# Performance work log

Hardware: AMD Instinct MI355X
Metric: run time of the kernel (lower is better)

Reference implementation:

```python
import jax, jax.numpy as jnp
import numpy as np

B, L, C, H, DK, MAXREL = 4, 1024, 768, 12, 64, 7
NEG = -2.0 ** 15  # masked_fill value


def _rel_pos_table(L, m):
    # abs distance, compressed logarithmically beyond m, clipped to [0, 2m]
    i = jnp.arange(L, dtype=jnp.float32)
    d = jnp.abs(i[:, None] - i[None, :])
    comp = m + jnp.log2(jnp.maximum(d - m, 1.0))
    d = jnp.where(d > m, comp, d)
    return jnp.clip(d, 0, 2 * m).astype(jnp.int32)  # [L, L]


def setup_inputs() -> dict:
    key = jax.random.key(0)
    ks = jax.random.split(key, 16)
    s = 0.02
    return {
        "qx": jax.random.normal(ks[0], (B, L, C), jnp.float32),
        "kx": jax.random.normal(ks[1], (B, L, C), jnp.float32),
        "vx": jax.random.normal(ks[2], (B, L, C), jnp.float32),
        "WQ_w": jax.random.normal(ks[3], (C, H * DK), jnp.float32) * s,
        "WQ_b": jnp.zeros((H * DK,), jnp.float32),
        "WK_w": jax.random.normal(ks[4], (C, H * DK), jnp.float32) * s,
        "WK_b": jnp.zeros((H * DK,), jnp.float32),
        "WV_w": jax.random.normal(ks[5], (C, H * DK), jnp.float32) * s,
        "WV_b": jnp.zeros((H * DK,), jnp.float32),
        "WO_w": jax.random.normal(ks[6], (H * DK, C), jnp.float32) * s,
        "WO_b": jnp.zeros((C,), jnp.float32),
        "embK": jax.random.normal(ks[7], (2 * MAXREL + 1, H), jnp.float32),
        "embB": jax.random.normal(ks[8], (2 * MAXREL + 1, H), jnp.float32) * s,
        "preScores": jax.random.normal(ks[9], (B, H, L, L), jnp.float32) * 0.1,
        "maskPAD": jnp.ones((B, L, L), jnp.int32),
    }


def reference(qx, kx, vx, WQ_w, WQ_b, WK_w, WK_b, WV_w, WV_b, WO_w, WO_b,
              embK, embB, preScores, maskPAD):
    q = (qx @ WQ_w + WQ_b).reshape(B, L, H, DK).transpose(0, 2, 1, 3)  # [B,H,L,dk]
    k = (kx @ WK_w + WK_b).reshape(B, L, H, DK).transpose(0, 2, 1, 3)
    v = (vx @ WV_w + WV_b).reshape(B, L, H, DK).transpose(0, 2, 1, 3)

    scores = jnp.einsum('bhid,bhjd->bhij', q, k) / np.sqrt(DK).astype(np.float32)

    tab = _rel_pos_table(L, MAXREL)                 # [L, L] int
    relK = jnp.transpose(embK[tab], (2, 1, 0))      # [H, L, L] (torch transpose(0,-1))
    relB = jnp.transpose(embB[tab], (2, 1, 0))
    scores = scores * relK[None] + relB[None]

    scores = scores + preScores
    scores = jnp.where((maskPAD == 0)[:, None, :, :], jnp.float32(NEG), scores)

    alpha = jax.nn.softmax(scores, axis=-1)         # dropout is identity in eval
    z = jnp.einsum('bhij,bhjd->bhid', alpha, v)     # [B,H,L,dk]
    z = z.transpose(0, 2, 1, 3).reshape(B, L, H * DK)
    z = z @ WO_w + WO_b
    return (z, scores)
```

## Files before the change

### kernel.cpp

```cpp
#include <hip/hip_runtime.h>
#include <stdint.h>


typedef __attribute__((ext_vector_type(4))) float f32x4;
typedef __attribute__((ext_vector_type(4))) int   i32x4;
typedef __attribute__((ext_vector_type(8))) short short8;
typedef __attribute__((ext_vector_type(4))) unsigned int u32x4;
typedef __attribute__((ext_vector_type(2))) unsigned int u32x2;

__device__ __forceinline__ unsigned short f2bf(float f) {
  unsigned int u = __float_as_uint(f);
  u += 0x7fffu + ((u >> 16) & 1u);
  return (unsigned short)(u >> 16);
}

__global__ __launch_bounds__(256) void conv_x_kernel(
    const float* __restrict__ qx, const float* __restrict__ kx,
    const float* __restrict__ vx, unsigned short* __restrict__ out) {
  int v = blockIdx.x * 256 + threadIdx.x;
  int mat = v / 786432;
  int r = v - mat * 786432;
  const float* src = (mat == 0) ? qx : (mat == 1) ? kx : vx;
  f32x4 x = ((const f32x4*)src)[r];
  union { unsigned short s[4]; u32x2 u; } o;
  o.s[0] = f2bf(x[0]); o.s[1] = f2bf(x[1]); o.s[2] = f2bf(x[2]); o.s[3] = f2bf(x[3]);
  ((u32x2*)out)[v] = o.u;
}

__global__ __launch_bounds__(256) void conv_mask_kernel(
    const int* __restrict__ m, unsigned int* __restrict__ out) {
  int w = blockIdx.x * 256 + threadIdx.x;
  const int* src = m + (size_t)w * 32;
  unsigned int bits = 0u;
#pragma unroll
  for (int c = 0; c < 8; c++) {
    i32x4 v = *(const i32x4*)&src[c * 4];
#pragma unroll
    for (int r = 0; r < 4; r++)
      bits |= (v[r] != 0 ? 1u : 0u) << (c * 4 + r);
  }
  out[w] = bits;
}

__global__ __launch_bounds__(256) void conv_w_kernel(
    const float* __restrict__ w0, const float* __restrict__ w1,
    const float* __restrict__ w2, const float* __restrict__ w3,
    unsigned short* __restrict__ out) {
  __shared__ float T[64][65];
  int bx = blockIdx.x;
  int mat = bx / 144; int t2 = bx - mat * 144;
  int kt = t2 / 12, nt = t2 - kt * 12;
  int k0 = kt * 64, n0 = nt * 64;
  const float* W = (mat == 0) ? w0 : (mat == 1) ? w1 : (mat == 2) ? w2 : w3;
  unsigned short* WT = out + (size_t)mat * 589824;
  int t = threadIdx.x;
  int lr = t >> 4;
  int lc = (t & 15) * 4;
#pragma unroll
  for (int p = 0; p < 4; p++) {
    int row = p * 16 + lr;
    f32x4 x = *(const f32x4*)&W[(size_t)(k0 + row) * 768 + n0 + lc];
    T[lc + 0][row] = x[0]; T[lc + 1][row] = x[1];
    T[lc + 2][row] = x[2]; T[lc + 3][row] = x[3];
  }
  __syncthreads();
#pragma unroll
  for (int p = 0; p < 4; p++) {
    int row = p * 16 + lr;
    union { unsigned short s[4]; u32x2 u; } o;
    o.s[0] = f2bf(T[row][lc + 0]); o.s[1] = f2bf(T[row][lc + 1]);
    o.s[2] = f2bf(T[row][lc + 2]); o.s[3] = f2bf(T[row][lc + 3]);
    *(u32x2*)&WT[(size_t)(n0 + row) * 768 + k0 + lc] = o.u;
  }
}

__global__ __launch_bounds__(256, 2) void qkv_gemm_kernel(
    const unsigned short* __restrict__ xbf, const unsigned short* __restrict__ wt,
    const float* __restrict__ bq, const float* __restrict__ bk, const float* __restrict__ bv,
    unsigned short* __restrict__ qo, unsigned short* __restrict__ ko,
    unsigned short* __restrict__ vto) {
  __shared__ unsigned short SM[2][2][128 * 72];
  int bx = blockIdx.x;
  int mat = bx / 192; int rem = bx - mat * 192;
  int mt = rem / 6, nt = rem - mt * 6;
  int m0 = mt * 128, n0 = nt * 128;
  const unsigned short* A = xbf + (size_t)mat * 4096 * 768;
  const unsigned short* Bm = wt + (size_t)mat * 768 * 768;
  int t = threadIdx.x;
  int wave = t >> 6, lane = t & 63;
  int wm = (wave >> 1) * 64, wn = (wave & 1) * 64;
  int col = lane & 15, quad = lane >> 4;
  int srow = t >> 3;
  int sch = (t & 7) * 8;

  f32x4 acc[4][4];
#pragma unroll
  for (int i = 0; i < 4; i++)
#pragma unroll
    for (int j = 0; j < 4; j++) acc[i][j] = (f32x4){0.f, 0.f, 0.f, 0.f};

  u32x4 ra[4], rb[4];
#pragma unroll
  for (int p = 0; p < 4; p++) {
    ra[p] = *(const u32x4*)&A[(size_t)(m0 + srow + p * 32) * 768 + sch];
    rb[p] = *(const u32x4*)&Bm[(size_t)(n0 + srow + p * 32) * 768 + sch];
  }
#pragma unroll
  for (int p = 0; p < 4; p++) {
    *(u32x4*)&SM[0][0][(srow + p * 32) * 72 + sch] = ra[p];
    *(u32x4*)&SM[0][1][(srow + p * 32) * 72 + sch] = rb[p];
  }
#pragma unroll
  for (int p = 0; p < 4; p++) {
    ra[p] = *(const u32x4*)&A[(size_t)(m0 + srow + p * 32) * 768 + 64 + sch];
    rb[p] = *(const u32x4*)&Bm[(size_t)(n0 + srow + p * 32) * 768 + 64 + sch];
  }
  __syncthreads();

  for (int it = 0; it < 12; ++it) {
    const unsigned short* As = SM[it & 1][0];
    const unsigned short* Bs = SM[it & 1][1];
#pragma unroll
    for (int c = 0; c < 2; c++) {
      short8 af[4], bf[4];
#pragma unroll
      for (int i = 0; i < 4; i++) {
        af[i] = *(const short8*)&As[(wm + i * 16 + col) * 72 + c * 32 + quad * 8];
        bf[i] = *(const short8*)&Bs[(wn + i * 16 + col) * 72 + c * 32 + quad * 8];
      }
#pragma unroll
      for (int i = 0; i < 4; i++)
#pragma unroll
        for (int j = 0; j < 4; j++)
          acc[i][j] = __builtin_amdgcn_mfma_f32_16x16x32_bf16(af[i], bf[j], acc[i][j], 0, 0, 0);
    }
    if (it < 11) {
      unsigned short* An = SM[(it + 1) & 1][0];
      unsigned short* Bn = SM[(it + 1) & 1][1];
#pragma unroll
      for (int p = 0; p < 4; p++) {
        *(u32x4*)&An[(srow + p * 32) * 72 + sch] = ra[p];
        *(u32x4*)&Bn[(srow + p * 32) * 72 + sch] = rb[p];
      }
      if (it < 10) {
        int kk2 = (it + 2) * 64;
#pragma unroll
        for (int p = 0; p < 4; p++) {
          ra[p] = *(const u32x4*)&A[(size_t)(m0 + srow + p * 32) * 768 + kk2 + sch];
          rb[p] = *(const u32x4*)&Bm[(size_t)(n0 + srow + p * 32) * 768 + kk2 + sch];
        }
      }
      __syncthreads();
    }
  }

  if (mat != 2) {
    const float* bias = (mat == 0) ? bq : bk;
    unsigned short* dst = (mat == 0) ? qo : ko;
#pragma unroll
    for (int j = 0; j < 4; j++) {
      int gn = n0 + wn + j * 16 + col;
      float bsv = bias[gn];
      int h = gn >> 6, d = gn & 63;
#pragma unroll
      for (int i = 0; i < 4; i++) {
#pragma unroll
        for (int r = 0; r < 4; r++) {
          int gm = m0 + wm + i * 16 + quad * 4 + r;
          int b = gm >> 10, l = gm & 1023;
          dst[((size_t)(b * 12 + h) * 1024 + l) * 64 + d] = f2bf(acc[i][j][r] + bsv);
        }
      }
    }
  } else {
    unsigned short* Tr = &SM[0][0][0];
    __syncthreads();
#pragma unroll
    for (int j = 0; j < 4; j++) {
      int n = wn + j * 16 + col;
      float bsv = bv[n0 + n];
#pragma unroll
      for (int i = 0; i < 4; i++) {
        int m = wm + i * 16 + quad * 4;
        union { unsigned short s[4]; u32x2 u; } pk;
#pragma unroll
        for (int r = 0; r < 4; r++) pk.s[r] = f2bf(acc[i][j][r] + bsv);
        *(u32x2*)&Tr[(size_t)n * 132 + m] = pk.u;
      }
    }
    __syncthreads();
#pragma unroll
    for (int p = 0; p < 8; p++) {
      int row = (t >> 4) + p * 16;
      int ch = (t & 15) * 8;
      u32x4 val = *(const u32x4*)&Tr[(size_t)row * 132 + ch];
      int gn = n0 + row;
      int h = gn >> 6, d = gn & 63;
      int gm = m0 + ch;
      int b = gm >> 10, l = gm & 1023;
      *(u32x4*)&vto[((size_t)(b * 12 + h) * 64 + d) * 1024 + l] = val;
    }
  }
}

__global__ __launch_bounds__(256, 3) void attn_kernel(
    const unsigned short* __restrict__ q, const unsigned short* __restrict__ k,
    const unsigned short* __restrict__ vt, const float* __restrict__ preS,
    const unsigned int* __restrict__ maskbits, const float* __restrict__ embK,
    const float* __restrict__ embB, float* __restrict__ scores,
    unsigned short* __restrict__ zpre) {
  __shared__ unsigned short Ks[128 * 72];
  __shared__ unsigned short Vs[64 * 136];
  __shared__ unsigned short Ps[64 * 136];
  __shared__ float eKs[16], eBs[16];
  int bx = blockIdx.x;
  int slice = bx % 48, it = bx / 48;
  int b = slice / 12, h = slice - b * 12;
  int i0 = it * 64;
  int t = threadIdx.x, wave = t >> 6, lane = t & 63;
  int col = lane & 15, quad = lane >> 4;

  if (t < 15) { eKs[t] = embK[t * 12 + h]; eBs[t] = embB[t * 12 + h]; }

  const unsigned short* qbase = q + ((size_t)(b * 12 + h) * 1024 + i0) * 64;
  const unsigned short* kbase = k + (size_t)(b * 12 + h) * 1024 * 64;
  const unsigned short* vbase = vt + (size_t)(b * 12 + h) * 64 * 1024;
  int lrow = wave * 16 + col;
  int gi = i0 + lrow;
  const float* prow = preS + ((size_t)(b * 12 + h) * 1024 + i0 + lrow) * 1024;
  float* srow_p = scores + ((size_t)(b * 12 + h) * 1024 + i0 + lrow) * 1024;
  const unsigned int* mrow = maskbits + ((size_t)(b * 1024 + i0 + lrow)) * 32;

  short8 qf[2];
  qf[0] = *(const short8*)&qbase[(size_t)lrow * 64 + quad * 8];
  qf[1] = *(const short8*)&qbase[(size_t)lrow * 64 + 32 + quad * 8];

  int kr = t >> 3, kc = (t & 7) * 8;
  int vr = t >> 4, vc = (t & 15) * 8;

  f32x4 oacc[4];
#pragma unroll
  for (int nd = 0; nd < 4; nd++) oacc[nd] = (f32x4){0.f, 0.f, 0.f, 0.f};
  float m_s = -3.0e38f, l_s = 0.f;

  u32x4 kvK[4], kvV[4];
#pragma unroll
  for (int p = 0; p < 4; p++) kvK[p] = *(const u32x4*)&kbase[(size_t)(kr + p * 32) * 64 + kc];
#pragma unroll
  for (int p = 0; p < 4; p++) kvV[p] = *(const u32x4*)&vbase[(size_t)(vr + p * 16) * 1024 + vc];
#pragma unroll
  for (int p = 0; p < 4; p++) *(u32x4*)&Ks[(kr + p * 32) * 72 + kc] = kvK[p];
#pragma unroll
  for (int p = 0; p < 4; p++) *(u32x4*)&Vs[(vr + p * 16) * 136 + vc] = kvV[p];
  f32x4 preC[8];
#pragma unroll
  for (int ns = 0; ns < 8; ns++)
    preC[ns] = *(const f32x4*)&prow[ns * 16 + quad * 4];
  u32x4 mkC = *(const u32x4*)&mrow[0];
#pragma unroll
  for (int p = 0; p < 4; p++) kvK[p] = *(const u32x4*)&kbase[(size_t)(128 + kr + p * 32) * 64 + kc];
#pragma unroll
  for (int p = 0; p < 4; p++) kvV[p] = *(const u32x4*)&vbase[(size_t)(vr + p * 16) * 1024 + 128 + vc];
  __syncthreads();

  for (int jt = 0; jt < 8; ++jt) {
    const int j0 = jt * 128;
    f32x4 sacc[8];
#pragma unroll
    for (int ns = 0; ns < 8; ns++) sacc[ns] = (f32x4){0.f, 0.f, 0.f, 0.f};
#pragma unroll
    for (int c = 0; c < 2; c++) {
#pragma unroll
      for (int ns = 0; ns < 8; ns++) {
        short8 kf = *(const short8*)&Ks[(ns * 16 + col) * 72 + c * 32 + quad * 8];
        sacc[ns] = __builtin_amdgcn_mfma_f32_16x16x32_bf16(kf, qf[c], sacc[ns], 0, 0, 0);
      }
    }
    float sv[8][4];
#pragma unroll
    for (int ns = 0; ns < 8; ns++) {
      int gj0 = j0 + ns * 16 + quad * 4;
      unsigned int hb = (mkC[ns >> 1] >> (((ns & 1) << 4) + (quad << 2))) & 0xFu;
      f32x4 sout;
#pragma unroll
      for (int r = 0; r < 4; r++) {
        int dd = gi - (gj0 + r); dd = dd < 0 ? -dd : dd;
        int idx;
        if (dd <= 7) idx = dd;
        else { idx = 38 - __clz(dd - 7); idx = idx > 14 ? 14 : idx; }
        float s = sacc[ns][r] * 0.125f * eKs[idx] + eBs[idx] + preC[ns][r];
        if (((hb >> r) & 1u) == 0u) s = -32768.0f;
        sout[r] = s; sv[ns][r] = s;
      }
      *(f32x4*)&srow_p[gj0] = sout;
    }
    float mx = sv[0][0];
#pragma unroll
    for (int ns = 0; ns < 8; ns++)
#pragma unroll
      for (int r = 0; r < 4; r++) mx = fmaxf(mx, sv[ns][r]);
    mx = fmaxf(mx, __shfl_xor(mx, 16));
    mx = fmaxf(mx, __shfl_xor(mx, 32));
    float mn = fmaxf(m_s, mx);
    float alpha = __expf(m_s - mn);
    float rs = 0.f;
#pragma unroll
    for (int ns = 0; ns < 8; ns++)
#pragma unroll
      for (int r = 0; r < 4; r++) { float p = __expf(sv[ns][r] - mn); sv[ns][r] = p; rs += p; }
    rs += __shfl_xor(rs, 16); rs += __shfl_xor(rs, 32);
    l_s = l_s * alpha + rs;
    m_s = mn;
#pragma unroll
    for (int nd = 0; nd < 4; nd++)
#pragma unroll
      for (int r = 0; r < 4; r++) oacc[nd][r] *= alpha;
#pragma unroll
    for (int ns = 0; ns < 8; ns++) {
      union { unsigned short s[4]; u32x2 u; } pk;
#pragma unroll
      for (int r = 0; r < 4; r++) pk.s[r] = f2bf(sv[ns][r]);
      *(u32x2*)&Ps[(size_t)lrow * 136 + ns * 16 + quad * 4] = pk.u;
    }
    if (jt < 7) {
#pragma unroll
      for (int ns = 0; ns < 8; ns++)
        preC[ns] = *(const f32x4*)&prow[j0 + 128 + ns * 16 + quad * 4];
      mkC = *(const u32x4*)&mrow[(jt + 1) * 4];
    }
#pragma unroll
    for (int c2 = 0; c2 < 4; c2++) {
      short8 pf = *(const short8*)&Ps[(wave * 16 + col) * 136 + c2 * 32 + quad * 8];
#pragma unroll
      for (int nd = 0; nd < 4; nd++) {
        short8 vf = *(const short8*)&Vs[(nd * 16 + col) * 136 + c2 * 32 + quad * 8];
        oacc[nd] = __builtin_amdgcn_mfma_f32_16x16x32_bf16(vf, pf, oacc[nd], 0, 0, 0);
      }
    }
    __syncthreads();
    if (jt < 7) {
#pragma unroll
      for (int p = 0; p < 4; p++) *(u32x4*)&Ks[(kr + p * 32) * 72 + kc] = kvK[p];
#pragma unroll
      for (int p = 0; p < 4; p++) *(u32x4*)&Vs[(vr + p * 16) * 136 + vc] = kvV[p];
      if (jt < 6) {
        int j2 = j0 + 256;
#pragma unroll
        for (int p = 0; p < 4; p++)
          kvK[p] = *(const u32x4*)&kbase[(size_t)(j2 + kr + p * 32) * 64 + kc];
#pragma unroll
        for (int p = 0; p < 4; p++)
          kvV[p] = *(const u32x4*)&vbase[(size_t)(vr + p * 16) * 1024 + j2 + vc];
      }
      __syncthreads();
    }
  }

  float inv = 1.0f / fmaxf(l_s, 1e-30f);
  unsigned short* zb = zpre + ((size_t)(b * 12 + h) * 1024 + i0 + lrow) * 64;
#pragma unroll
  for (int nd = 0; nd < 4; nd++) {
    union { unsigned short s[4]; u32x2 u; } zk;
#pragma unroll
    for (int r = 0; r < 4; r++) zk.s[r] = f2bf(oacc[nd][r] * inv);
    *(u32x2*)&zb[nd * 16 + quad * 4] = zk.u;
  }
}

__global__ __launch_bounds__(256, 3) void out_gemm_kernel(
    const unsigned short* __restrict__ zpre, const unsigned short* __restrict__ wot,
    const float* __restrict__ wob, float* __restrict__ zout) {
  __shared__ unsigned short SM[2][2][64 * 72];
  int bx = blockIdx.x;
  int mt = bx / 12, nt = bx - mt * 12;
  int m0 = mt * 64, n0 = nt * 64;
  int t = threadIdx.x;
  int wave = t >> 6, lane = t & 63;
  int wm = (wave >> 1) * 32, wn = (wave & 1) * 32;
  int col = lane & 15, quad = lane >> 4;
  int srow = t >> 3, sch = (t & 7) * 8;
  int gmA0 = m0 + srow, gmA1 = m0 + srow + 32;
  int bA0 = gmA0 >> 10, lA0 = gmA0 & 1023;
  int bA1 = gmA1 >> 10, lA1 = gmA1 & 1023;

  f32x4 acc[2][2];
#pragma unroll
  for (int i = 0; i < 2; i++)
#pragma unroll
    for (int j = 0; j < 2; j++) acc[i][j] = (f32x4){0.f, 0.f, 0.f, 0.f};

  u32x4 ra[2], rb[2];
  ra[0] = *(const u32x4*)&zpre[((size_t)(bA0 * 12 + 0) * 1024 + lA0) * 64 + sch];
  ra[1] = *(const u32x4*)&zpre[((size_t)(bA1 * 12 + 0) * 1024 + lA1) * 64 + sch];
  rb[0] = *(const u32x4*)&wot[(size_t)(n0 + srow) * 768 + sch];
  rb[1] = *(const u32x4*)&wot[(size_t)(n0 + srow + 32) * 768 + sch];
  *(u32x4*)&SM[0][0][srow * 72 + sch] = ra[0];
  *(u32x4*)&SM[0][0][(srow + 32) * 72 + sch] = ra[1];
  *(u32x4*)&SM[0][1][srow * 72 + sch] = rb[0];
  *(u32x4*)&SM[0][1][(srow + 32) * 72 + sch] = rb[1];
  ra[0] = *(const u32x4*)&zpre[((size_t)(bA0 * 12 + 1) * 1024 + lA0) * 64 + sch];
  ra[1] = *(const u32x4*)&zpre[((size_t)(bA1 * 12 + 1) * 1024 + lA1) * 64 + sch];
  rb[0] = *(const u32x4*)&wot[(size_t)(n0 + srow) * 768 + 64 + sch];
  rb[1] = *(const u32x4*)&wot[(size_t)(n0 + srow + 32) * 768 + 64 + sch];
  __syncthreads();

  for (int it = 0; it < 12; ++it) {
    const unsigned short* As = SM[it & 1][0];
    const unsigned short* Bs = SM[it & 1][1];
#pragma unroll
    for (int c = 0; c < 2; c++) {
      short8 af[2], bf[2];
#pragma unroll
      for (int i = 0; i < 2; i++) {
        af[i] = *(const short8*)&As[(wm + i * 16 + col) * 72 + c * 32 + quad * 8];
        bf[i] = *(const short8*)&Bs[(wn + i * 16 + col) * 72 + c * 32 + quad * 8];
      }
#pragma unroll
      for (int i = 0; i < 2; i++)
#pragma unroll
        for (int j = 0; j < 2; j++)
          acc[i][j] = __builtin_amdgcn_mfma_f32_16x16x32_bf16(af[i], bf[j], acc[i][j], 0, 0, 0);
    }
    if (it < 11) {
      unsigned short* An = SM[(it + 1) & 1][0];
      unsigned short* Bn = SM[(it + 1) & 1][1];
      *(u32x4*)&An[srow * 72 + sch] = ra[0];
      *(u32x4*)&An[(srow + 32) * 72 + sch] = ra[1];
      *(u32x4*)&Bn[srow * 72 + sch] = rb[0];
      *(u32x4*)&Bn[(srow + 32) * 72 + sch] = rb[1];
      if (it < 10) {
        int hh = it + 2;
        ra[0] = *(const u32x4*)&zpre[((size_t)(bA0 * 12 + hh) * 1024 + lA0) * 64 + sch];
        ra[1] = *(const u32x4*)&zpre[((size_t)(bA1 * 12 + hh) * 1024 + lA1) * 64 + sch];
        rb[0] = *(const u32x4*)&wot[(size_t)(n0 + srow) * 768 + hh * 64 + sch];
        rb[1] = *(const u32x4*)&wot[(size_t)(n0 + srow + 32) * 768 + hh * 64 + sch];
      }
      __syncthreads();
    }
  }
#pragma unroll
  for (int j = 0; j < 2; j++) {
    int gn = n0 + wn + j * 16 + col;
    float bsv = wob[gn];
#pragma unroll
    for (int i = 0; i < 2; i++) {
#pragma unroll
      for (int r = 0; r < 4; r++) {
        int gm = m0 + wm + i * 16 + quad * 4 + r;
        zout[(size_t)gm * 768 + gn] = acc[i][j][r] + bsv;
      }
    }
  }
}

extern "C" void kernel_launch(void* const* d_in, const int* in_sizes, int n_in,
                              void* d_out, int out_size, void* d_ws, size_t ws_size,
                              hipStream_t stream) {
  const float* qx   = (const float*)d_in[0];
  const float* kx   = (const float*)d_in[1];
  const float* vx   = (const float*)d_in[2];
  const float* WQ_w = (const float*)d_in[3];
  const float* WQ_b = (const float*)d_in[4];
  const float* WK_w = (const float*)d_in[5];
  const float* WK_b = (const float*)d_in[6];
  const float* WV_w = (const float*)d_in[7];
  const float* WV_b = (const float*)d_in[8];
  const float* WO_w = (const float*)d_in[9];
  const float* WO_b = (const float*)d_in[10];
  const float* embK = (const float*)d_in[11];
  const float* embB = (const float*)d_in[12];
  const float* preS = (const float*)d_in[13];
  const int* maskP  = (const int*)d_in[14];

  float* zout = (float*)d_out;
  float* scores = zout + 3145728;
  unsigned short* xbf = (unsigned short*)scores;
  unsigned int* mbits = (unsigned int*)zout;

  char* ws = (char*)d_ws;
  unsigned short* wt  = (unsigned short*)(ws);
  unsigned short* qb  = (unsigned short*)(ws + 4718592);
  unsigned short* kb  = (unsigned short*)(ws + 11010048);
  unsigned short* vtb = (unsigned short*)(ws + 17301504);
  unsigned short* zp  = (unsigned short*)(ws + 23592960);

  conv_x_kernel<<<9216, 256, 0, stream>>>(qx, kx, vx, xbf);
  conv_mask_kernel<<<512, 256, 0, stream>>>(maskP, mbits);
  conv_w_kernel<<<576, 256, 0, stream>>>(WQ_w, WK_w, WV_w, WO_w, wt);
  qkv_gemm_kernel<<<576, 256, 0, stream>>>(xbf, wt, WQ_b, WK_b, WV_b, qb, kb, vtb);
  attn_kernel<<<768, 256, 0, stream>>>(qb, kb, vtb, preS, mbits, embK, embB, scores, zp);
  out_gemm_kernel<<<192 * 4, 256, 0, stream>>>(zp, wt + 3 * 589824, WO_b, zout);
}
```

Baseline: 479.9 us.

## Read K/V fragments directly from global memory and single-buffer QKV GEMM LDS

The attention kernel no longer stages K and V tiles through shared memory. Each wave now loads its MFMA operand fragments straight from global memory, relying on L1/L2 to serve the repeated reads. This removes the LDS traffic and two block barriers per tile, and the lower LDS use allows a higher occupancy bound. The QKV GEMM drops to a single LDS buffer with an extra barrier per k-step, also to allow more blocks per CU. The cost is that every wave re-fetches K/V from cache with uncoalesced 16-byte loads and no prefetch, which exposes global latency inside the MFMA loop.

```diff
diff --git a/kernel.cpp b/kernel.cpp
--- a/kernel.cpp
+++ b/kernel.cpp
@@ -74,12 +74,12 @@
   }
 }
 
-__global__ __launch_bounds__(256, 2) void qkv_gemm_kernel(
+__global__ __launch_bounds__(256, 3) void qkv_gemm_kernel(
     const unsigned short* __restrict__ xbf, const unsigned short* __restrict__ wt,
     const float* __restrict__ bq, const float* __restrict__ bk, const float* __restrict__ bv,
     unsigned short* __restrict__ qo, unsigned short* __restrict__ ko,
     unsigned short* __restrict__ vto) {
-  __shared__ unsigned short SM[2][2][128 * 72];
+  __shared__ unsigned short SM[2][128 * 72];
   int bx = blockIdx.x;
   int mat = bx / 192; int rem = bx - mat * 192;
   int mt = rem / 6, nt = rem - mt * 6;
@@ -107,8 +107,8 @@
   }
 #pragma unroll
   for (int p = 0; p < 4; p++) {
-    *(u32x4*)&SM[0][0][(srow + p * 32) * 72 + sch] = ra[p];
-    *(u32x4*)&SM[0][1][(srow + p * 32) * 72 + sch] = rb[p];
+    *(u32x4*)&SM[0][(srow + p * 32) * 72 + sch] = ra[p];
+    *(u32x4*)&SM[1][(srow + p * 32) * 72 + sch] = rb[p];
   }
 #pragma unroll
   for (int p = 0; p < 4; p++) {
@@ -118,8 +118,8 @@
   __syncthreads();
 
   for (int it = 0; it < 12; ++it) {
-    const unsigned short* As = SM[it & 1][0];
-    const unsigned short* Bs = SM[it & 1][1];
+    const unsigned short* As = SM[0];
+    const unsigned short* Bs = SM[1];
 #pragma unroll
     for (int c = 0; c < 2; c++) {
       short8 af[4], bf[4];
@@ -135,12 +135,11 @@
           acc[i][j] = __builtin_amdgcn_mfma_f32_16x16x32_bf16(af[i], bf[j], acc[i][j], 0, 0, 0);
     }
     if (it < 11) {
-      unsigned short* An = SM[(it + 1) & 1][0];
-      unsigned short* Bn = SM[(it + 1) & 1][1];
+      __syncthreads();
 #pragma unroll
       for (int p = 0; p < 4; p++) {
-        *(u32x4*)&An[(srow + p * 32) * 72 + sch] = ra[p];
-        *(u32x4*)&Bn[(srow + p * 32) * 72 + sch] = rb[p];
+        *(u32x4*)&SM[0][(srow + p * 32) * 72 + sch] = ra[p];
+        *(u32x4*)&SM[1][(srow + p * 32) * 72 + sch] = rb[p];
       }
       if (it < 10) {
         int kk2 = (it + 2) * 64;
@@ -173,7 +172,7 @@
       }
     }
   } else {
-    unsigned short* Tr = &SM[0][0][0];
+    unsigned short* Tr = &SM[0][0];
     __syncthreads();
 #pragma unroll
     for (int j = 0; j < 4; j++) {
@@ -203,14 +202,12 @@
   }
 }
 
-__global__ __launch_bounds__(256, 3) void attn_kernel(
+__global__ __launch_bounds__(256, 4) void attn_kernel(
     const unsigned short* __restrict__ q, const unsigned short* __restrict__ k,
     const unsigned short* __restrict__ vt, const float* __restrict__ preS,
     const unsigned int* __restrict__ maskbits, const float* __restrict__ embK,
     const float* __restrict__ embB, float* __restrict__ scores,
     unsigned short* __restrict__ zpre) {
-  __shared__ unsigned short Ks[128 * 72];
-  __shared__ unsigned short Vs[64 * 136];
   __shared__ unsigned short Ps[64 * 136];
   __shared__ float eKs[16], eBs[16];
   int bx = blockIdx.x;
@@ -221,6 +218,7 @@
   int col = lane & 15, quad = lane >> 4;
 
   if (t < 15) { eKs[t] = embK[t * 12 + h]; eBs[t] = embB[t * 12 + h]; }
+  __syncthreads();
 
   const unsigned short* qbase = q + ((size_t)(b * 12 + h) * 1024 + i0) * 64;
   const unsigned short* kbase = k + (size_t)(b * 12 + h) * 1024 * 64;
@@ -235,33 +233,16 @@
   qf[0] = *(const short8*)&qbase[(size_t)lrow * 64 + quad * 8];
   qf[1] = *(const short8*)&qbase[(size_t)lrow * 64 + 32 + quad * 8];
 
-  int kr = t >> 3, kc = (t & 7) * 8;
-  int vr = t >> 4, vc = (t & 15) * 8;
-
   f32x4 oacc[4];
 #pragma unroll
   for (int nd = 0; nd < 4; nd++) oacc[nd] = (f32x4){0.f, 0.f, 0.f, 0.f};
   float m_s = -3.0e38f, l_s = 0.f;
 
-  u32x4 kvK[4], kvV[4];
-#pragma unroll
-  for (int p = 0; p < 4; p++) kvK[p] = *(const u32x4*)&kbase[(size_t)(kr + p * 32) * 64 + kc];
-#pragma unroll
-  for (int p = 0; p < 4; p++) kvV[p] = *(const u32x4*)&vbase[(size_t)(vr + p * 16) * 1024 + vc];
-#pragma unroll
-  for (int p = 0; p < 4; p++) *(u32x4*)&Ks[(kr + p * 32) * 72 + kc] = kvK[p];
-#pragma unroll
-  for (int p = 0; p < 4; p++) *(u32x4*)&Vs[(vr + p * 16) * 136 + vc] = kvV[p];
   f32x4 preC[8];
 #pragma unroll
   for (int ns = 0; ns < 8; ns++)
     preC[ns] = *(const f32x4*)&prow[ns * 16 + quad * 4];
   u32x4 mkC = *(const u32x4*)&mrow[0];
-#pragma unroll
-  for (int p = 0; p < 4; p++) kvK[p] = *(const u32x4*)&kbase[(size_t)(128 + kr + p * 32) * 64 + kc];
-#pragma unroll
-  for (int p = 0; p < 4; p++) kvV[p] = *(const u32x4*)&vbase[(size_t)(vr + p * 16) * 1024 + 128 + vc];
-  __syncthreads();
 
   for (int jt = 0; jt < 8; ++jt) {
     const int j0 = jt * 128;
@@ -272,7 +253,7 @@
     for (int c = 0; c < 2; c++) {
 #pragma unroll
       for (int ns = 0; ns < 8; ns++) {
-        short8 kf = *(const short8*)&Ks[(ns * 16 + col) * 72 + c * 32 + quad * 8];
+        short8 kf = *(const short8*)&kbase[(size_t)(j0 + ns * 16 + col) * 64 + c * 32 + quad * 8];
         sacc[ns] = __builtin_amdgcn_mfma_f32_16x16x32_bf16(kf, qf[c], sacc[ns], 0, 0, 0);
       }
     }
@@ -333,26 +314,9 @@
       short8 pf = *(const short8*)&Ps[(wave * 16 + col) * 136 + c2 * 32 + quad * 8];
 #pragma unroll
       for (int nd = 0; nd < 4; nd++) {
-        short8 vf = *(const short8*)&Vs[(nd * 16 + col) * 136 + c2 * 32 + quad * 8];
+        short8 vf = *(const short8*)&vbase[(size_t)(nd * 16 + col) * 1024 + j0 + c2 * 32 + quad * 8];
         oacc[nd] = __builtin_amdgcn_mfma_f32_16x16x32_bf16(vf, pf, oacc[nd], 0, 0, 0);
       }
-    }
-    __syncthreads();
-    if (jt < 7) {
-#pragma unroll
-      for (int p = 0; p < 4; p++) *(u32x4*)&Ks[(kr + p * 32) * 72 + kc] = kvK[p];
-#pragma unroll
-      for (int p = 0; p < 4; p++) *(u32x4*)&Vs[(vr + p * 16) * 136 + vc] = kvV[p];
-      if (jt < 6) {
-        int j2 = j0 + 256;
-#pragma unroll
-        for (int p = 0; p < 4; p++)
-          kvK[p] = *(const u32x4*)&kbase[(size_t)(j2 + kr + p * 32) * 64 + kc];
-#pragma unroll
-        for (int p = 0; p < 4; p++)
-          kvV[p] = *(const u32x4*)&vbase[(size_t)(vr + p * 16) * 1024 + j2 + vc];
-      }
-      __syncthreads();
     }
   }
 
```

Measured after the change: 608.4 us. 1.27x slower.
